# Performance work log

Hardware: AMD Instinct MI355X
Metric: run time of the kernel (lower is better)

Reference implementation:

```python
import jax, jax.numpy as jnp
import numpy as np

N_NODES = 100000
N_EDGES = 3200000
N_GRAPHS = 512
F_IN = 256
HID = 16
N_CLS = 8


def setup_inputs() -> dict:
    key = jax.random.key(0)
    ks = jax.random.split(key, 6)
    x = jax.random.normal(ks[0], (N_NODES, F_IN), jnp.float32)
    edge_index = jax.random.randint(ks[1], (2, N_EDGES), 0, N_NODES, dtype=jnp.int64)
    batch = jnp.sort(jax.random.randint(ks[2], (N_NODES,), 0, N_GRAPHS, dtype=jnp.int64))
    W1 = jax.random.normal(ks[3], (F_IN, HID), jnp.float32) / np.float32(np.sqrt(F_IN))
    b1 = jnp.zeros((HID,), jnp.float32)
    W2 = jax.random.normal(ks[4], (HID, N_CLS), jnp.float32) / np.float32(np.sqrt(HID))
    b2 = jnp.zeros((N_CLS,), jnp.float32)
    return {"x": x, "edge_index": edge_index, "batch": batch, "num_graphs": N_GRAPHS,
            "W1": W1, "b1": b1, "W2": W2, "b2": b2}


def _gcn_conv(x, src, dst, W, b, n):
    # PyG GCNConv: linear transform, then sym-normalized scatter-add (self-loops
    # already appended to src/dst by caller), bias added after aggregation.
    h = x @ W  # [N, out]
    deg = jax.ops.segment_sum(jnp.ones_like(dst, h.dtype), dst, num_segments=n)
    dinv = jax.lax.rsqrt(jnp.maximum(deg, 1.0))  # deg >= 1 due to self-loops
    norm = dinv[src] * dinv[dst]  # [E+N]
    out = jax.ops.segment_sum(h[src] * norm[:, None], dst, num_segments=n)
    return out + b


def reference(x, edge_index, batch, num_graphs, W1, b1, W2, b2):
    n = x.shape[0]
    loop = jnp.arange(n, dtype=edge_index.dtype)
    src = jnp.concatenate([edge_index[0], loop])
    dst = jnp.concatenate([edge_index[1], loop])
    h = jax.nn.relu(_gcn_conv(x, src, dst, W1, b1, n))
    h = _gcn_conv(h, src, dst, W2, b2, n)
    # global mean pool over graphs
    sums = jax.ops.segment_sum(h, batch, num_segments=num_graphs)
    cnt = jax.ops.segment_sum(jnp.ones((n,), h.dtype), batch, num_segments=num_graphs)
    return sums / jnp.maximum(cnt, 1.0)[:, None]
```

## Files before the change

kernel.cpp:

```cpp
#include <hip/hip_runtime.h>

#define F_IN 256
#define HID 16
#define NCLS 8
#define BSH 9
#define NPB 512
#define MAXBINS 256
#define BCAP 18432u
#define TILE 4096
#define WIN 8
#define GROWS 64
#define APITCH 280

typedef float f4v __attribute__((ext_vector_type(4)));
typedef float f32x4 __attribute__((ext_vector_type(4)));
typedef _Float16 h2v __attribute__((ext_vector_type(2)));
typedef _Float16 f16x4 __attribute__((ext_vector_type(4)));
typedef _Float16 f16x8 __attribute__((ext_vector_type(8)));

__global__ void k_bininit(unsigned* __restrict__ binCur, int nbins) {
    int t = threadIdx.x;
    if (t < nbins) binCur[t] = (unsigned)t * BCAP;
}

__global__ void __launch_bounds__(256) k_binA(const int* __restrict__ src,
                                              const int* __restrict__ dst, int e,
                                              unsigned* __restrict__ binCur,
                                              unsigned* __restrict__ binbuf) {
    __shared__ unsigned scnt[MAXBINS], lbase[MAXBINS], gbase[MAXBINS];
    __shared__ unsigned sbuf[TILE];
    __shared__ unsigned char sbin[TILE];
    int t = threadIdx.x;
    if (t < MAXBINS) scnt[t] = 0u;
    __syncthreads();
    int base = blockIdx.x * TILE;
    unsigned ent[16], rank[16];
    int ebin[16];
#pragma unroll
    for (int i = 0; i < 16; ++i) {
        int j = base + t + i * 256;
        ebin[i] = -1;
        if (j < e) {
            int d = __builtin_nontemporal_load(&dst[j]);
            int s = __builtin_nontemporal_load(&src[j]);
            ent[i] = ((unsigned)s << BSH) | ((unsigned)d & (NPB - 1));
            ebin[i] = d >> BSH;
            rank[i] = atomicAdd(&scnt[ebin[i]], 1u);
        }
    }
    __syncthreads();
    if (t == 0) {
        unsigned run = 0;
        for (int b = 0; b < MAXBINS; ++b) { lbase[b] = run; run += scnt[b]; }
    }
    __syncthreads();
    if (t < MAXBINS && scnt[t] > 0u) gbase[t] = atomicAdd(&binCur[t], scnt[t]);
    __syncthreads();
#pragma unroll
    for (int i = 0; i < 16; ++i)
        if (ebin[i] >= 0) {
            unsigned p = lbase[ebin[i]] + rank[i];
            sbuf[p] = ent[i];
            sbin[p] = (unsigned char)ebin[i];
        }
    __syncthreads();
    int total = e - base; if (total > TILE) total = TILE;
    for (int idx = t; idx < total; idx += 256) {
        int b = sbin[idx];
        __builtin_nontemporal_store(sbuf[idx], &binbuf[gbase[b] + ((unsigned)idx - lbase[b])]);
    }
}

__global__ void __launch_bounds__(256) k_binB(const unsigned* __restrict__ binbuf,
                                              const unsigned* __restrict__ binCur,
                                              int n,
                                              unsigned* __restrict__ srcs,
                                              unsigned* __restrict__ off,
                                              unsigned* __restrict__ degc) {
    __shared__ unsigned hist[NPB];
    __shared__ unsigned pref[NPB];
    __shared__ unsigned s1[256];
    int t = threadIdx.x;
    int b = blockIdx.x;
    unsigned base = (unsigned)b * BCAP;
    unsigned end = binCur[b];
    for (int i = t; i < NPB; i += 256) hist[i] = 0u;
    __syncthreads();
    for (unsigned j = base + t; j < end; j += 256)
        atomicAdd(&hist[__builtin_nontemporal_load(&binbuf[j]) & (NPB - 1)], 1u);
    __syncthreads();
    unsigned h0 = hist[2 * t], h1 = hist[2 * t + 1];
    unsigned pair = h0 + h1;
    s1[t] = pair;
    __syncthreads();
    for (int o = 1; o < 256; o <<= 1) {
        unsigned v = (t >= o) ? s1[t - o] : 0u;
        __syncthreads();
        s1[t] += v;
        __syncthreads();
    }
    unsigned exc = s1[t] - pair;
    pref[2 * t] = exc;
    pref[2 * t + 1] = exc + h0;
    __syncthreads();
    int dbase = b << BSH;
    for (int i = t; i < NPB; i += 256) {
        int d = dbase + i;
        if (d < n) { off[d] = base + pref[i]; degc[d] = hist[i]; }
    }
    __syncthreads();
    for (int i = t; i < NPB; i += 256) hist[i] = 0u;
    __syncthreads();
    for (unsigned j = base + t; j < end; j += 256) {
        unsigned v = __builtin_nontemporal_load(&binbuf[j]);
        unsigned dl = v & (NPB - 1);
        unsigned r = atomicAdd(&hist[dl], 1u);
        srcs[base + pref[dl] + r] = v >> BSH;
    }
}

__global__ void __launch_bounds__(256) k_gemm1(const float* __restrict__ x,
                                               const float* __restrict__ W1,
                                               const unsigned* __restrict__ degc,
                                               _Float16* __restrict__ t1h, int n) {
    __shared__ _Float16 xs[4][16 * APITCH];
    int t = threadIdx.x;
    int lane = t & 63;
    int wv = t >> 6;
    int col = lane & 15;
    int k0 = (lane >> 4) * 8;
    f16x8 bfrag[8];
#pragma unroll
    for (int kc = 0; kc < 8; ++kc)
#pragma unroll
        for (int j = 0; j < 8; ++j)
            bfrag[kc][j] = (_Float16)W1[(kc * 32 + k0 + j) * HID + col];
    int rbase = blockIdx.x * GROWS;
    int nrows = n - rbase; if (nrows > GROWS) nrows = GROWS;
#pragma unroll
    for (int it = 0; it < GROWS * 64 / 256; ++it) {
        int q = t + it * 256;
        int row = q >> 6, c4 = q & 63;
        if (row < nrows) {
            f4v v = __builtin_nontemporal_load(
                &((const f4v*)(x + (size_t)(rbase + row) * F_IN))[c4]);
            f16x4 hv;
            hv[0] = (_Float16)v[0]; hv[1] = (_Float16)v[1];
            hv[2] = (_Float16)v[2]; hv[3] = (_Float16)v[3];
            *(f16x4*)&xs[row >> 4][(row & 15) * APITCH + c4 * 4] = hv;
        }
    }
    __syncthreads();
    f32x4 acc = {0.f, 0.f, 0.f, 0.f};
    const _Float16* tile = xs[wv];
    int arow = lane & 15;
#pragma unroll
    for (int kc = 0; kc < 8; ++kc) {
        f16x8 afrag = *(const f16x8*)&tile[arow * APITCH + kc * 32 + k0];
        acc = __builtin_amdgcn_mfma_f32_16x16x32_f16(afrag, bfrag[kc], acc, 0, 0, 0);
    }
    int r0 = (lane >> 4) * 4;
#pragma unroll
    for (int reg = 0; reg < 4; ++reg) {
        int grow = rbase + wv * 16 + r0 + reg;
        if (grow < n) {
            float v = acc[reg] * rsqrtf((float)(degc[grow] + 1u));
            t1h[(size_t)grow * HID + col] = (_Float16)v;
        }
    }
}

__global__ void __launch_bounds__(256) k_agg1(const unsigned* __restrict__ srcs,
                                              const unsigned* __restrict__ off,
                                              const unsigned* __restrict__ degc,
                                              const unsigned* __restrict__ t1h,
                                              const float* __restrict__ b1,
                                              unsigned* __restrict__ hbuf, int n) {
    int t = threadIdx.x;
    int d = blockIdx.x * 16 + (t >> 4);
    if (d >= n) return;
    int lane8 = t & 7;
    int oct = (t >> 3) & 1;
    unsigned p = off[d];
    unsigned c = degc[d];
    float a0 = 0.f, a1 = 0.f;
    union { unsigned u; h2v h; } cv;
    unsigned i = oct;
    for (; i + 2 < c; i += 4) {
        unsigned sA = srcs[p + i];
        unsigned sB = srcs[p + i + 2];
        unsigned wA = t1h[(size_t)sA * 8 + lane8];
        unsigned wB = t1h[(size_t)sB * 8 + lane8];
        cv.u = wA; a0 += (float)cv.h[0]; a1 += (float)cv.h[1];
        cv.u = wB; a0 += (float)cv.h[0]; a1 += (float)cv.h[1];
    }
    if (i < c) {
        unsigned w = t1h[(size_t)srcs[p + i] * 8 + lane8];
        cv.u = w; a0 += (float)cv.h[0]; a1 += (float)cv.h[1];
    }
    a0 += __shfl_xor(a0, 8, 64);
    a1 += __shfl_xor(a1, 8, 64);
    if (oct == 0) {
        cv.u = t1h[(size_t)d * 8 + lane8];
        a0 += (float)cv.h[0]; a1 += (float)cv.h[1];
        float di = rsqrtf((float)(c + 1u));
        float h0 = fmaxf(di * a0 + b1[2 * lane8], 0.f);
        float h1 = fmaxf(di * a1 + b1[2 * lane8 + 1], 0.f);
        union { unsigned u; h2v h; } pk;
        pk.h[0] = (_Float16)h0; pk.h[1] = (_Float16)h1;
        hbuf[(size_t)d * 8 + lane8] = pk.u;
    }
}

__global__ void __launch_bounds__(256) k_gemm2(const unsigned* __restrict__ hbuf,
                                               const float* __restrict__ W2,
                                               const unsigned* __restrict__ degc,
                                               unsigned* __restrict__ t2h, int n) {
    __shared__ float w2s[HID * NCLS];
    if (threadIdx.x < HID * NCLS) w2s[threadIdx.x] = W2[threadIdx.x];
    __syncthreads();
    int i = blockIdx.x * 256 + threadIdx.x;
    if (i >= n) return;
    union { uint4 q; unsigned u[4]; } A, B;
    const uint4* hb = (const uint4*)(hbuf + (size_t)i * 8);
    A.q = hb[0]; B.q = hb[1];
    float h[HID];
    union { unsigned u; h2v h; } cv;
#pragma unroll
    for (int q = 0; q < 4; ++q) {
        cv.u = A.u[q]; h[2 * q] = (float)cv.h[0]; h[2 * q + 1] = (float)cv.h[1];
        cv.u = B.u[q]; h[8 + 2 * q] = (float)cv.h[0]; h[8 + 2 * q + 1] = (float)cv.h[1];
    }
    float o[NCLS];
#pragma unroll
    for (int c = 0; c < NCLS; ++c) o[c] = 0.f;
#pragma unroll
    for (int k = 0; k < HID; ++k)
#pragma unroll
        for (int c = 0; c < NCLS; ++c) o[c] += h[k] * w2s[k * NCLS + c];
    float di = rsqrtf((float)(degc[i] + 1u));
    union { uint4 q; unsigned u[4]; } O;
#pragma unroll
    for (int q = 0; q < 4; ++q) {
        union { unsigned u; h2v h; } pk;
        pk.h[0] = (_Float16)(o[2 * q] * di);
        pk.h[1] = (_Float16)(o[2 * q + 1] * di);
        O.u[q] = pk.u;
    }
    ((uint4*)(t2h + (size_t)i * 4))[0] = O.q;
}

__global__ void __launch_bounds__(256) k_agg2pool(const unsigned* __restrict__ srcs,
                                                  const unsigned* __restrict__ off,
                                                  const unsigned* __restrict__ degc,
                                                  const unsigned* __restrict__ t2h,
                                                  const float* __restrict__ b2,
                                                  const int* __restrict__ batch,
                                                  float* __restrict__ out,
                                                  float* __restrict__ cg, int n) {
    __shared__ float wacc[WIN * NCLS];
    __shared__ float wcnt[WIN];
    __shared__ int gb_s;
    int t = threadIdx.x;
    int bbase = blockIdx.x * 32;
    if (t < WIN * NCLS) wacc[t] = 0.f;
    if (t < WIN) wcnt[t] = 0.f;
    if (t == 0) gb_s = batch[bbase < n ? bbase : (n - 1)];
    __syncthreads();
    int d = bbase + (t >> 3);
    int lane4 = t & 3;
    int pr = (t >> 2) & 1;
    if (d < n) {
        unsigned p = off[d];
        unsigned c = degc[d];
        float a0 = 0.f, a1 = 0.f;
        union { unsigned u; h2v h; } cv;
        unsigned i = pr;
        for (; i + 2 < c; i += 4) {
            unsigned wA = t2h[(size_t)srcs[p + i] * 4 + lane4];
            unsigned wB = t2h[(size_t)srcs[p + i + 2] * 4 + lane4];
            cv.u = wA; a0 += (float)cv.h[0]; a1 += (float)cv.h[1];
            cv.u = wB; a0 += (float)cv.h[0]; a1 += (float)cv.h[1];
        }
        if (i < c) {
            unsigned w = t2h[(size_t)srcs[p + i] * 4 + lane4];
            cv.u = w; a0 += (float)cv.h[0]; a1 += (float)cv.h[1];
        }
        a0 += __shfl_xor(a0, 4, 64);
        a1 += __shfl_xor(a1, 4, 64);
        if (pr == 0) {
            cv.u = t2h[(size_t)d * 4 + lane4];
            a0 += (float)cv.h[0]; a1 += (float)cv.h[1];
            float di = rsqrtf((float)(c + 1u));
            float v0 = di * a0 + b2[2 * lane4];
            float v1 = di * a1 + b2[2 * lane4 + 1];
            int g = batch[d];
            int gi = g - gb_s;
            if (gi < WIN) {
                atomicAdd(&wacc[gi * NCLS + 2 * lane4], v0);
                atomicAdd(&wacc[gi * NCLS + 2 * lane4 + 1], v1);
                if ((t & 7) == 0) atomicAdd(&wcnt[gi], 1.f);
            } else {
                atomicAdd(&out[(size_t)g * NCLS + 2 * lane4], v0);
                atomicAdd(&out[(size_t)g * NCLS + 2 * lane4 + 1], v1);
                if ((t & 7) == 0) atomicAdd(&cg[g], 1.f);
            }
        }
    }
    __syncthreads();
    if (t < WIN * NCLS && wcnt[t >> 3] > 0.f)
        atomicAdd(&out[(size_t)(gb_s + (t >> 3)) * NCLS + (t & 7)], wacc[t]);
    if (t < WIN && wcnt[t] > 0.f) atomicAdd(&cg[gb_s + t], wcnt[t]);
}

__global__ void k_div(float* __restrict__ out, const float* __restrict__ cg, int total) {
    int i = blockIdx.x * blockDim.x + threadIdx.x;
    if (i < total) out[i] /= fmaxf(cg[i / NCLS], 1.0f);
}

extern "C" void kernel_launch(void* const* d_in, const int* in_sizes, int n_in,
                              void* d_out, int out_size, void* d_ws, size_t ws_size,
                              hipStream_t stream) {
    const float* x = (const float*)d_in[0];
    const int* ei = (const int*)d_in[1];
    const int* batch = (const int*)d_in[2];
    const float* W1 = (const float*)d_in[4];
    const float* b1 = (const float*)d_in[5];
    const float* W2 = (const float*)d_in[6];
    const float* b2 = (const float*)d_in[7];

    int n = in_sizes[0] / F_IN;
    int e = in_sizes[1] / 2;
    int g = out_size / NCLS;
    const int* src = ei;
    const int* dst = ei + e;
    int nbins = (n + NPB - 1) >> BSH;

    char* w = (char*)d_ws;
    unsigned* binCur = (unsigned*)w; w += (size_t)MAXBINS * 4;
    unsigned* degc   = (unsigned*)w; w += (size_t)n * 4;
    unsigned* off    = (unsigned*)w; w += (size_t)n * 4;
    unsigned* t1h    = (unsigned*)w; w += (size_t)n * 8 * 4;
    unsigned* hbuf   = (unsigned*)w; w += (size_t)n * 8 * 4;
    unsigned* t2h    = (unsigned*)w; w += (size_t)n * 4 * 4;
    float* cg        = (float*)w;    w += (size_t)g * 4;
    w = (char*)(((size_t)w + 255) & ~(size_t)255);
    unsigned* binbuf = (unsigned*)w; w += (size_t)nbins * BCAP * 4;
    unsigned* srcs   = (unsigned*)w; w += (size_t)nbins * BCAP * 4;

    hipMemsetAsync(cg, 0, (size_t)g * 4, stream);
    hipMemsetAsync(d_out, 0, (size_t)out_size * 4, stream);

    k_bininit<<<1, 256, 0, stream>>>(binCur, nbins);
    k_binA<<<(e + TILE - 1) / TILE, 256, 0, stream>>>(src, dst, e, binCur, binbuf);
    k_binB<<<nbins, 256, 0, stream>>>(binbuf, binCur, n, srcs, off, degc);
    k_gemm1<<<(n + GROWS - 1) / GROWS, 256, 0, stream>>>(x, W1, degc, (_Float16*)t1h, n);
    k_agg1<<<(n + 15) / 16, 256, 0, stream>>>(srcs, off, degc, t1h, b1, hbuf, n);
    k_gemm2<<<(n + 255) / 256, 256, 0, stream>>>(hbuf, W2, degc, t2h, n);
    k_agg2pool<<<(n + 31) / 32, 256, 0, stream>>>(srcs, off, degc, t2h, b2, batch,
                                                  (float*)d_out, cg, n);
    k_div<<<(out_size + 255) / 256, 256, 0, stream>>>((float*)d_out, cg, out_size);
}
```

Measured before the change: 197.0 us.

## Enlarge binning tile, prepack W1 fragments, unroll gather loops deeper

Three separate changes. The edge-binning kernel now runs 512 threads over 8192-edge tiles, halving the block count and the global atomics on bin cursors. The W1 fp16 MFMA fragments are packed once in the init kernel, so each gemm1 block does vector loads instead of 64 strided scalar converts. Both aggregation kernels gain an 8-wide unrolled gather loop to keep more independent loads in flight. The larger shared-memory tile and higher register use may reduce occupancy.

```diff
diff --git a/kernel.cpp b/kernel.cpp
--- a/kernel.cpp
+++ b/kernel.cpp
@@ -7,7 +7,7 @@
 #define NPB 512
 #define MAXBINS 256
 #define BCAP 18432u
-#define TILE 4096
+#define TILE 8192
 #define WIN 8
 #define GROWS 64
 #define APITCH 280
@@ -18,12 +18,24 @@
 typedef _Float16 f16x4 __attribute__((ext_vector_type(4)));
 typedef _Float16 f16x8 __attribute__((ext_vector_type(8)));
 
-__global__ void k_bininit(unsigned* __restrict__ binCur, int nbins) {
+__global__ void k_init(unsigned* __restrict__ binCur, int nbins,
+                       const float* __restrict__ W1, _Float16* __restrict__ wfrag) {
     int t = threadIdx.x;
     if (t < nbins) binCur[t] = (unsigned)t * BCAP;
-}
-
-__global__ void __launch_bounds__(256) k_binA(const int* __restrict__ src,
+    if (t < 64) {
+        int col = t & 15, k0 = (t >> 4) * 8;
+#pragma unroll
+        for (int kc = 0; kc < 8; ++kc) {
+            f16x8 v;
+#pragma unroll
+            for (int j = 0; j < 8; ++j)
+                v[j] = (_Float16)W1[(kc * 32 + k0 + j) * HID + col];
+            *(f16x8*)&wfrag[((size_t)t * 8 + kc) * 8] = v;
+        }
+    }
+}
+
+__global__ void __launch_bounds__(512) k_binA(const int* __restrict__ src,
                                               const int* __restrict__ dst, int e,
                                               unsigned* __restrict__ binCur,
                                               unsigned* __restrict__ binbuf) {
@@ -38,7 +50,7 @@
     int ebin[16];
 #pragma unroll
     for (int i = 0; i < 16; ++i) {
-        int j = base + t + i * 256;
+        int j = base + t + i * 512;
         ebin[i] = -1;
         if (j < e) {
             int d = __builtin_nontemporal_load(&dst[j]);
@@ -65,7 +77,7 @@
         }
     __syncthreads();
     int total = e - base; if (total > TILE) total = TILE;
-    for (int idx = t; idx < total; idx += 256) {
+    for (int idx = t; idx < total; idx += 512) {
         int b = sbin[idx];
         __builtin_nontemporal_store(sbuf[idx], &binbuf[gbase[b] + ((unsigned)idx - lbase[b])]);
     }
@@ -120,7 +132,7 @@
 }
 
 __global__ void __launch_bounds__(256) k_gemm1(const float* __restrict__ x,
-                                               const float* __restrict__ W1,
+                                               const _Float16* __restrict__ wfrag,
                                                const unsigned* __restrict__ degc,
                                                _Float16* __restrict__ t1h, int n) {
     __shared__ _Float16 xs[4][16 * APITCH];
@@ -132,9 +144,7 @@
     f16x8 bfrag[8];
 #pragma unroll
     for (int kc = 0; kc < 8; ++kc)
-#pragma unroll
-        for (int j = 0; j < 8; ++j)
-            bfrag[kc][j] = (_Float16)W1[(kc * 32 + k0 + j) * HID + col];
+        bfrag[kc] = *(const f16x8*)&wfrag[((size_t)lane * 8 + kc) * 8];
     int rbase = blockIdx.x * GROWS;
     int nrows = n - rbase; if (nrows > GROWS) nrows = GROWS;
 #pragma unroll
@@ -186,13 +196,24 @@
     float a0 = 0.f, a1 = 0.f;
     union { unsigned u; h2v h; } cv;
     unsigned i = oct;
+    for (; i + 6 < c; i += 8) {
+        unsigned s0 = srcs[p + i],     s1 = srcs[p + i + 2];
+        unsigned s2 = srcs[p + i + 4], s3 = srcs[p + i + 6];
+        unsigned w0 = t1h[(size_t)s0 * 8 + lane8];
+        unsigned w1 = t1h[(size_t)s1 * 8 + lane8];
+        unsigned w2 = t1h[(size_t)s2 * 8 + lane8];
+        unsigned w3 = t1h[(size_t)s3 * 8 + lane8];
+        cv.u = w0; a0 += (float)cv.h[0]; a1 += (float)cv.h[1];
+        cv.u = w1; a0 += (float)cv.h[0]; a1 += (float)cv.h[1];
+        cv.u = w2; a0 += (float)cv.h[0]; a1 += (float)cv.h[1];
+        cv.u = w3; a0 += (float)cv.h[0]; a1 += (float)cv.h[1];
+    }
     for (; i + 2 < c; i += 4) {
-        unsigned sA = srcs[p + i];
-        unsigned sB = srcs[p + i + 2];
-        unsigned wA = t1h[(size_t)sA * 8 + lane8];
-        unsigned wB = t1h[(size_t)sB * 8 + lane8];
-        cv.u = wA; a0 += (float)cv.h[0]; a1 += (float)cv.h[1];
-        cv.u = wB; a0 += (float)cv.h[0]; a1 += (float)cv.h[1];
+        unsigned s0 = srcs[p + i], s1 = srcs[p + i + 2];
+        unsigned w0 = t1h[(size_t)s0 * 8 + lane8];
+        unsigned w1 = t1h[(size_t)s1 * 8 + lane8];
+        cv.u = w0; a0 += (float)cv.h[0]; a1 += (float)cv.h[1];
+        cv.u = w1; a0 += (float)cv.h[0]; a1 += (float)cv.h[1];
     }
     if (i < c) {
         unsigned w = t1h[(size_t)srcs[p + i] * 8 + lane8];
@@ -276,11 +297,21 @@
         float a0 = 0.f, a1 = 0.f;
         union { unsigned u; h2v h; } cv;
         unsigned i = pr;
+        for (; i + 6 < c; i += 8) {
+            unsigned w0 = t2h[(size_t)srcs[p + i] * 4 + lane4];
+            unsigned w1 = t2h[(size_t)srcs[p + i + 2] * 4 + lane4];
+            unsigned w2 = t2h[(size_t)srcs[p + i + 4] * 4 + lane4];
+            unsigned w3 = t2h[(size_t)srcs[p + i + 6] * 4 + lane4];
+            cv.u = w0; a0 += (float)cv.h[0]; a1 += (float)cv.h[1];
+            cv.u = w1; a0 += (float)cv.h[0]; a1 += (float)cv.h[1];
+            cv.u = w2; a0 += (float)cv.h[0]; a1 += (float)cv.h[1];
+            cv.u = w3; a0 += (float)cv.h[0]; a1 += (float)cv.h[1];
+        }
         for (; i + 2 < c; i += 4) {
-            unsigned wA = t2h[(size_t)srcs[p + i] * 4 + lane4];
-            unsigned wB = t2h[(size_t)srcs[p + i + 2] * 4 + lane4];
-            cv.u = wA; a0 += (float)cv.h[0]; a1 += (float)cv.h[1];
-            cv.u = wB; a0 += (float)cv.h[0]; a1 += (float)cv.h[1];
+            unsigned w0 = t2h[(size_t)srcs[p + i] * 4 + lane4];
+            unsigned w1 = t2h[(size_t)srcs[p + i + 2] * 4 + lane4];
+            cv.u = w0; a0 += (float)cv.h[0]; a1 += (float)cv.h[1];
+            cv.u = w1; a0 += (float)cv.h[0]; a1 += (float)cv.h[1];
         }
         if (i < c) {
             unsigned w = t2h[(size_t)srcs[p + i] * 4 + lane4];
@@ -343,6 +374,7 @@
     unsigned* t1h    = (unsigned*)w; w += (size_t)n * 8 * 4;
     unsigned* hbuf   = (unsigned*)w; w += (size_t)n * 8 * 4;
     unsigned* t2h    = (unsigned*)w; w += (size_t)n * 4 * 4;
+    _Float16* wfrag  = (_Float16*)w; w += (size_t)64 * 8 * 8 * 2;
     float* cg        = (float*)w;    w += (size_t)g * 4;
     w = (char*)(((size_t)w + 255) & ~(size_t)255);
     unsigned* binbuf = (unsigned*)w; w += (size_t)nbins * BCAP * 4;
@@ -351,10 +383,10 @@
     hipMemsetAsync(cg, 0, (size_t)g * 4, stream);
     hipMemsetAsync(d_out, 0, (size_t)out_size * 4, stream);
 
-    k_bininit<<<1, 256, 0, stream>>>(binCur, nbins);
-    k_binA<<<(e + TILE - 1) / TILE, 256, 0, stream>>>(src, dst, e, binCur, binbuf);
+    k_init<<<1, 256, 0, stream>>>(binCur, nbins, W1, wfrag);
+    k_binA<<<(e + TILE - 1) / TILE, 512, 0, stream>>>(src, dst, e, binCur, binbuf);
     k_binB<<<nbins, 256, 0, stream>>>(binbuf, binCur, n, srcs, off, degc);
-    k_gemm1<<<(n + GROWS - 1) / GROWS, 256, 0, stream>>>(x, W1, degc, (_Float16*)t1h, n);
+    k_gemm1<<<(n + GROWS - 1) / GROWS, 256, 0, stream>>>(x, wfrag, degc, (_Float16*)t1h, n);
     k_agg1<<<(n + 15) / 16, 256, 0, stream>>>(srcs, off, degc, t1h, b1, hbuf, n);
     k_gemm2<<<(n + 255) / 256, 256, 0, stream>>>(hbuf, W2, degc, t2h, n);
     k_agg2pool<<<(n + 31) / 32, 256, 0, stream>>>(srcs, off, degc, t2h, b2, batch,
```

Result: faster. 188.1 us (-4.5%).
